# Performance work log

Hardware: AMD Instinct MI355X
Metric: run time of the kernel (lower is better)

## Reference

```python
import jax, jax.numpy as jnp
import numpy as np

B, T, F = 2048, 60, 89
H = 1024
OUT = 30  # output_predicted_chords


def setup_inputs() -> dict:
    key = jax.random.key(0)
    k1, k2, k3, k4 = jax.random.split(key, 4)
    # small init scale keeps the relu-activated recurrence numerically stable
    s = 0.02
    return {
        "x": jax.random.normal(k1, (B, T, F), dtype=jnp.float32),
        "W": jax.random.normal(k2, (F, 4 * H), dtype=jnp.float32) * s,
        "U": jax.random.normal(k3, (H, 4 * H), dtype=jnp.float32) * s,
        "b": jnp.zeros((4 * H,), dtype=jnp.float32),
        "Wd": jax.random.normal(k4, (H, OUT), dtype=jnp.float32) * s,
        "bd": jnp.zeros((OUT,), dtype=jnp.float32),
    }


def _lstm_last_h(x, W, U, b):
    """Keras LSTM(activation='relu', recurrent_activation='sigmoid').
    Gate order in Keras kernels: i, f, c (candidate), o.
    Returns last hidden state h_T of shape [B, H]."""
    Bsz = x.shape[0]
    Hdim = U.shape[0]
    # precompute input projections for all timesteps: [T, B, 4H]
    xz = jnp.einsum('btf,fg->tbg', x, W) + b

    def step(carry, xz_t):
        h, c = carry
        z = xz_t + h @ U                      # [B, 4H]
        i, f, g, o = jnp.split(z, 4, axis=-1)
        i = jax.nn.sigmoid(i)
        f = jax.nn.sigmoid(f)
        g = jax.nn.relu(g)                    # activation='relu' on candidate
        o = jax.nn.sigmoid(o)
        c = f * c + i * g
        h = o * jax.nn.relu(c)                # activation='relu' on cell output
        return (h, c), None

    h0 = jnp.zeros((Bsz, Hdim), dtype=x.dtype)
    c0 = jnp.zeros((Bsz, Hdim), dtype=x.dtype)
    (hT, _), _ = jax.lax.scan(step, (h0, c0), xz)
    return hT


def reference(x, W, U, b, Wd, bd):
    # LSTM(return_sequences=True) then take x[:, -1, :] == last hidden state
    hT = _lstm_last_h(x, W, U, b)             # [B, H]
    y = hT @ Wd + bd                           # [B, OUT]
    return y.reshape(-1, OUT, 1)               # [B, 30, 1]
```

## Files before the change

### kernel.cpp

```cpp
#include <hip/hip_runtime.h>
#include <cstdint>
#include <cstddef>

#define Bsz 2048
#define Tseq 60
#define Fin 89
#define Hd 1024
#define G4 4096
#define KXP 128
#define NOUT 30

typedef _Float16 half8 __attribute__((ext_vector_type(8)));
typedef float f32x4 __attribute__((ext_vector_type(4)));

__device__ __forceinline__ void gload_lds16(const void* g, void* l) {
  __builtin_amdgcn_global_load_lds((const __attribute__((address_space(1))) void*)g,
                                   (__attribute__((address_space(3))) void*)l,
                                   16, 0, 0);
}

__device__ __forceinline__ float sigmoidf_fast(float x) {
  return 1.0f / (1.0f + __expf(-x));
}


__global__ __launch_bounds__(256) void convert_x(const float* __restrict__ x,
                                                 _Float16* __restrict__ xp) {
  int idx = blockIdx.x * 256 + threadIdx.x;
  int k = idx % KXP;
  int b = (idx / KXP) % Bsz;
  int t = idx / (KXP * Bsz);
  float v = (k < Fin) ? x[((size_t)b * Tseq + t) * Fin + k] : 0.0f;
  xp[idx] = (_Float16)v;
}

__global__ __launch_bounds__(256) void transpose_W(const float* __restrict__ W,
                                                   _Float16* __restrict__ Wpt) {
  __shared__ float tile[32][33];
  int n0 = blockIdx.x * 32;
  int k0 = blockIdx.y * 32;
  int tx = threadIdx.x, ty = threadIdx.y;
  for (int i = ty; i < 32; i += 8) {
    int k = k0 + i;
    tile[i][tx] = (k < Fin) ? W[(size_t)k * G4 + n0 + tx] : 0.0f;
  }
  __syncthreads();
  for (int i = ty; i < 32; i += 8)
    Wpt[(size_t)(n0 + i) * KXP + k0 + tx] = (_Float16)tile[tx][i];
}

__global__ __launch_bounds__(256) void transpose_U(const float* __restrict__ U,
                                                   _Float16* __restrict__ Upt) {
  __shared__ float tile[32][33];
  int n0 = blockIdx.x * 32;
  int k0 = blockIdx.y * 32;
  int tx = threadIdx.x, ty = threadIdx.y;
  for (int i = ty; i < 32; i += 8)
    tile[i][tx] = U[(size_t)(k0 + i) * G4 + n0 + tx];
  __syncthreads();
  for (int i = ty; i < 32; i += 8)
    Upt[(size_t)(n0 + i) * Hd + k0 + tx] = (_Float16)tile[tx][i];
}

__global__ __launch_bounds__(256, 2) void lstm_step(
    const _Float16* __restrict__ xp_t,
    const _Float16* __restrict__ Wpt,
    const _Float16* __restrict__ Upt,
    const float*    __restrict__ bias,
    const _Float16* __restrict__ h_in,
    _Float16*       __restrict__ h_out,
    float*          __restrict__ cst,
    int skip_h)
{
  __shared__ __align__(16) _Float16 As[2 * 8192];
  __shared__ __align__(16) _Float16 Bs[2 * 8192];

  const int tid  = threadIdx.x;
  const int wave = tid >> 6;
  const int lane = tid & 63;
  const int quad = lane >> 4;
  const int l16  = lane & 15;

  const int id  = blockIdx.x;
  const int xcd = id & 7, loc = id >> 3;
  const int m0 = (((xcd & 1) << 3) + (loc & 7)) * 128;
  const int j0 = (((xcd >> 1) << 3) + (loc >> 3)) * 32;

  const int srow = lane >> 2;
  const int qg   = (lane & 3) ^ ((lane >> 3) & 3);
  const int sA   = quad ^ ((l16 >> 1) & 3);

  const int hb    = 16 * (wave & 1);
  const int mwave = 64 * (wave >> 1);
  const int j  = j0 + hb + l16;
  const int uA = 4 * (wave >> 1);
  const int uB = wave & 1;
  const int aoff = l16 * 32 + sA * 8;

  float bv[4];
  for (int p = 0; p < 4; ++p) bv[p] = bias[p * Hd + j];

  f32x4 acc[4][4];
  for (int mi = 0; mi < 4; ++mi)
    for (int p = 0; p < 4; ++p)
      acc[mi][p] = f32x4{bv[p], bv[p], bv[p], bv[p]};

  auto stage = [&](int buf, int r) {
    const _Float16* Ab; const _Float16* Bb; int strA, strB, k0;
    if (r < 2) { Ab = xp_t; strA = KXP; Bb = Wpt; strB = KXP; k0 = r * 64; }
    else       { Ab = h_in; strA = Hd;  Bb = Upt; strB = Hd;  k0 = (r - 2) * 64; }
    _Float16* Ad = &As[buf * 8192];
    _Float16* Bd = &Bs[buf * 8192];
#pragma unroll
    for (int ii = 0; ii < 4; ++ii) {
      int i = ii * 4 + wave;
      int st = i >> 3, ci = i & 7;
      gload_lds16(Ab + (size_t)(m0 + ci * 16 + srow) * strA + k0 + st * 32 + qg * 8,
                  Ad + st * 4096 + ci * 512);
    }
#pragma unroll
    for (int ii = 0; ii < 4; ++ii) {
      int i = ii * 4 + wave;
      int st = i >> 3, ci = i & 7;
      int ln = ci * 16 + srow;
      int gn = (ln >> 5) * Hd + j0 + (ln & 31);
      gload_lds16(Bb + (size_t)gn * strB + k0 + st * 32 + qg * 8,
                  Bd + st * 4096 + ci * 512);
    }
  };

  auto compute = [&](int buf) {
    const __attribute__((address_space(3))) _Float16* As3 =
        (const __attribute__((address_space(3))) _Float16*)&As[buf * 8192];
    const __attribute__((address_space(3))) _Float16* Bs3 =
        (const __attribute__((address_space(3))) _Float16*)&Bs[buf * 8192];
    half8 a0[4], b0[4], a1[4], b1[4];
#pragma unroll
    for (int mi = 0; mi < 4; ++mi)
      asm volatile("ds_read_b128 %0, %1" : "=v"(a0[mi])
                   : "v"(As3 + (uA + mi) * 512 + aoff) : "memory");
#pragma unroll
    for (int p = 0; p < 4; ++p)
      asm volatile("ds_read_b128 %0, %1" : "=v"(b0[p])
                   : "v"(Bs3 + (2 * p + uB) * 512 + aoff) : "memory");
#pragma unroll
    for (int mi = 0; mi < 4; ++mi)
      asm volatile("ds_read_b128 %0, %1" : "=v"(a1[mi])
                   : "v"(As3 + 4096 + (uA + mi) * 512 + aoff) : "memory");
#pragma unroll
    for (int p = 0; p < 4; ++p)
      asm volatile("ds_read_b128 %0, %1" : "=v"(b1[p])
                   : "v"(Bs3 + 4096 + (2 * p + uB) * 512 + aoff) : "memory");
    asm volatile("s_waitcnt lgkmcnt(8)" ::: "memory");
    __builtin_amdgcn_sched_barrier(0);
#pragma unroll
    for (int mi = 0; mi < 4; ++mi)
#pragma unroll
      for (int p = 0; p < 4; ++p)
        acc[mi][p] = __builtin_amdgcn_mfma_f32_16x16x32_f16(a0[mi], b0[p],
                                                            acc[mi][p], 0, 0, 0);
    asm volatile("s_waitcnt lgkmcnt(0)" ::: "memory");
    __builtin_amdgcn_sched_barrier(0);
#pragma unroll
    for (int mi = 0; mi < 4; ++mi)
#pragma unroll
      for (int p = 0; p < 4; ++p)
        acc[mi][p] = __builtin_amdgcn_mfma_f32_16x16x32_f16(a1[mi], b1[p],
                                                            acc[mi][p], 0, 0, 0);
  };

  const int NR = skip_h ? 2 : 18;

  stage(0, 0);
  stage(1, 1);
  for (int r = 0; r < NR; ++r) {
    const int cur = r & 1;
    if (r < NR - 1) {
      asm volatile("s_waitcnt vmcnt(8)" ::: "memory");
    } else {
      asm volatile("s_waitcnt vmcnt(0)" ::: "memory");
    }
    __builtin_amdgcn_sched_barrier(0);
    __builtin_amdgcn_s_barrier();
    __builtin_amdgcn_s_setprio(1);
    compute(cur);
    __builtin_amdgcn_s_setprio(0);
    __builtin_amdgcn_s_barrier();
    if (r + 2 < NR) stage(cur, r + 2);
  }

  for (int mi = 0; mi < 4; ++mi) {
    for (int r = 0; r < 4; ++r) {
      int row = m0 + mwave + mi * 16 + quad * 4 + r;
      size_t idx = (size_t)row * Hd + j;
      float iv = sigmoidf_fast(acc[mi][0][r]);
      float fv = sigmoidf_fast(acc[mi][1][r]);
      float gv = fmaxf(acc[mi][2][r], 0.0f);
      float ov = sigmoidf_fast(acc[mi][3][r]);
      float cprev = skip_h ? 0.0f : cst[idx];
      float cv = fv * cprev + iv * gv;
      cst[idx] = cv;
      float hv = ov * fmaxf(cv, 0.0f);
      h_out[idx] = (_Float16)hv;
    }
  }
}

__global__ __launch_bounds__(256) void final_dense(const _Float16* __restrict__ h,
                                                   const float* __restrict__ Wd,
                                                   const float* __restrict__ bd,
                                                   float* __restrict__ y) {
  __shared__ float hs[Hd];
  __shared__ float red[8][32];
  int bi = blockIdx.x;
  for (int k = threadIdx.x; k < Hd; k += 256)
    hs[k] = (float)h[(size_t)bi * Hd + k];
  __syncthreads();
  int o  = threadIdx.x & 31;
  int ch = threadIdx.x >> 5;
  float p = 0.0f;
  if (o < NOUT) {
    int k0 = ch * (Hd / 8);
    for (int k = k0; k < k0 + (Hd / 8); ++k)
      p += hs[k] * Wd[(size_t)k * NOUT + o];
  }
  red[ch][o] = p;
  __syncthreads();
  if (threadIdx.x < NOUT) {
    float s = bd[threadIdx.x];
    for (int c2 = 0; c2 < 8; ++c2) s += red[c2][threadIdx.x];
    y[(size_t)bi * NOUT + threadIdx.x] = s;
  }
}


extern "C" void kernel_launch(void* const* d_in, const int* in_sizes, int n_in,
                              void* d_out, int out_size, void* d_ws, size_t ws_size,
                              hipStream_t stream) {
  const float* x  = (const float*)d_in[0];
  const float* W  = (const float*)d_in[1];
  const float* U  = (const float*)d_in[2];
  const float* b  = (const float*)d_in[3];
  const float* Wd = (const float*)d_in[4];
  const float* bd = (const float*)d_in[5];
  float* y = (float*)d_out;

  char* ws = (char*)d_ws;
  _Float16* xp  = (_Float16*)ws; ws += (size_t)Tseq * Bsz * KXP * 2;
  _Float16* Wpt = (_Float16*)ws; ws += (size_t)G4 * KXP * 2;
  _Float16* Upt = (_Float16*)ws; ws += (size_t)G4 * Hd * 2;
  _Float16* hb0 = (_Float16*)ws; ws += (size_t)Bsz * Hd * 2;
  _Float16* hb1 = (_Float16*)ws; ws += (size_t)Bsz * Hd * 2;
  float*    cst = (float*)ws;    ws += (size_t)Bsz * Hd * 4;

  convert_x<<<(Tseq * Bsz * KXP) / 256, 256, 0, stream>>>(x, xp);
  transpose_W<<<dim3(G4 / 32, KXP / 32), dim3(32, 8), 0, stream>>>(W, Wpt);
  transpose_U<<<dim3(G4 / 32, Hd / 32), dim3(32, 8), 0, stream>>>(U, Upt);

  for (int t = 0; t < Tseq; ++t) {
    const _Float16* hin  = ((t - 1) & 1) ? hb1 : hb0;
    _Float16*       hout = (t & 1) ? hb1 : hb0;
    lstm_step<<<dim3((Bsz / 128) * (G4 / 128)), 256, 0, stream>>>(
        xp + (size_t)t * (Bsz * KXP), Wpt, Upt, b,
        (t == 0) ? hb0 : hin, hout, cst, (t == 0) ? 1 : 0);
  }

  final_dense<<<Bsz, 256, 0, stream>>>(hb1, Wd, bd, y);
}
```

Before: 1.723 ms.

## Enlarge LSTM step tile to 128x256 with 8 waves and triple-buffered LDS

Each block now computes a 128-row by 256-gate-column tile (64 hidden units times 4 gates) with 512 threads, halving the grid to 256 blocks. The B operand tile doubles, so each A tile loaded into LDS is reused across twice as many columns. The LDS pipeline moves from double to triple buffering, with vmcnt waits adjusted to the new in-flight load counts. This cuts redundant global reads of h and x per step and gives the loads more latency hiding. In exchange it needs more LDS per block (144 KB), allows only one block per CU, and leaves 256 blocks for the machine's CUs, so wave-level parallelism is lower.

```diff
diff --git a/kernel.cpp b/kernel.cpp
--- a/kernel.cpp
+++ b/kernel.cpp
@@ -62,7 +62,7 @@
     Upt[(size_t)(n0 + i) * Hd + k0 + tx] = (_Float16)tile[tx][i];
 }
 
-__global__ __launch_bounds__(256, 2) void lstm_step(
+__global__ __launch_bounds__(512, 1) void lstm_step(
     const _Float16* __restrict__ xp_t,
     const _Float16* __restrict__ Wpt,
     const _Float16* __restrict__ Upt,
@@ -72,8 +72,8 @@
     float*          __restrict__ cst,
     int skip_h)
 {
-  __shared__ __align__(16) _Float16 As[2 * 8192];
-  __shared__ __align__(16) _Float16 Bs[2 * 8192];
+  __shared__ __align__(16) _Float16 As[3 * 8192];
+  __shared__ __align__(16) _Float16 Bs[3 * 16384];
 
   const int tid  = threadIdx.x;
   const int wave = tid >> 6;
@@ -83,25 +83,28 @@
 
   const int id  = blockIdx.x;
   const int xcd = id & 7, loc = id >> 3;
-  const int m0 = (((xcd & 1) << 3) + (loc & 7)) * 128;
-  const int j0 = (((xcd >> 1) << 3) + (loc >> 3)) * 32;
+  const int jpanel = 4 * (xcd & 3) + (loc & 3);
+  const int mpanel = 8 * (xcd >> 2) + (loc >> 2);
+  const int m0 = mpanel * 128;
+  const int j0 = jpanel * 64;
 
   const int srow = lane >> 2;
   const int qg   = (lane & 3) ^ ((lane >> 3) & 3);
   const int sA   = quad ^ ((l16 >> 1) & 3);
 
-  const int hb    = 16 * (wave & 1);
-  const int mwave = 64 * (wave >> 1);
-  const int j  = j0 + hb + l16;
-  const int uA = 4 * (wave >> 1);
-  const int uB = wave & 1;
+  const int mhalf = wave >> 2;
+  const int nq    = wave & 3;
+  const int j  = j0 + 16 * nq + l16;
   const int aoff = l16 * 32 + sA * 8;
 
   float bv[4];
+#pragma unroll
   for (int p = 0; p < 4; ++p) bv[p] = bias[p * Hd + j];
 
   f32x4 acc[4][4];
+#pragma unroll
   for (int mi = 0; mi < 4; ++mi)
+#pragma unroll
     for (int p = 0; p < 4; ++p)
       acc[mi][p] = f32x4{bv[p], bv[p], bv[p], bv[p]};
 
@@ -110,22 +113,21 @@
     if (r < 2) { Ab = xp_t; strA = KXP; Bb = Wpt; strB = KXP; k0 = r * 64; }
     else       { Ab = h_in; strA = Hd;  Bb = Upt; strB = Hd;  k0 = (r - 2) * 64; }
     _Float16* Ad = &As[buf * 8192];
-    _Float16* Bd = &Bs[buf * 8192];
-#pragma unroll
-    for (int ii = 0; ii < 4; ++ii) {
-      int i = ii * 4 + wave;
+    _Float16* Bd = &Bs[buf * 16384];
+#pragma unroll
+    for (int ii = 0; ii < 2; ++ii) {
+      int i = ii * 8 + wave;
       int st = i >> 3, ci = i & 7;
       gload_lds16(Ab + (size_t)(m0 + ci * 16 + srow) * strA + k0 + st * 32 + qg * 8,
                   Ad + st * 4096 + ci * 512);
     }
 #pragma unroll
     for (int ii = 0; ii < 4; ++ii) {
-      int i = ii * 4 + wave;
-      int st = i >> 3, ci = i & 7;
-      int ln = ci * 16 + srow;
-      int gn = (ln >> 5) * Hd + j0 + (ln & 31);
+      int i = ii * 8 + wave;
+      int st = i >> 4, ci = i & 15;
+      int gn = (ci >> 2) * Hd + j0 + 16 * (ci & 3) + srow;
       gload_lds16(Bb + (size_t)gn * strB + k0 + st * 32 + qg * 8,
-                  Bd + st * 4096 + ci * 512);
+                  Bd + st * 8192 + ci * 512);
     }
   };
 
@@ -133,24 +135,24 @@
     const __attribute__((address_space(3))) _Float16* As3 =
         (const __attribute__((address_space(3))) _Float16*)&As[buf * 8192];
     const __attribute__((address_space(3))) _Float16* Bs3 =
-        (const __attribute__((address_space(3))) _Float16*)&Bs[buf * 8192];
+        (const __attribute__((address_space(3))) _Float16*)&Bs[buf * 16384];
     half8 a0[4], b0[4], a1[4], b1[4];
 #pragma unroll
     for (int mi = 0; mi < 4; ++mi)
       asm volatile("ds_read_b128 %0, %1" : "=v"(a0[mi])
-                   : "v"(As3 + (uA + mi) * 512 + aoff) : "memory");
+                   : "v"(As3 + (4 * mhalf + mi) * 512 + aoff) : "memory");
 #pragma unroll
     for (int p = 0; p < 4; ++p)
       asm volatile("ds_read_b128 %0, %1" : "=v"(b0[p])
-                   : "v"(Bs3 + (2 * p + uB) * 512 + aoff) : "memory");
+                   : "v"(Bs3 + (4 * p + nq) * 512 + aoff) : "memory");
 #pragma unroll
     for (int mi = 0; mi < 4; ++mi)
       asm volatile("ds_read_b128 %0, %1" : "=v"(a1[mi])
-                   : "v"(As3 + 4096 + (uA + mi) * 512 + aoff) : "memory");
+                   : "v"(As3 + 4096 + (4 * mhalf + mi) * 512 + aoff) : "memory");
 #pragma unroll
     for (int p = 0; p < 4; ++p)
       asm volatile("ds_read_b128 %0, %1" : "=v"(b1[p])
-                   : "v"(Bs3 + 4096 + (2 * p + uB) * 512 + aoff) : "memory");
+                   : "v"(Bs3 + 8192 + (4 * p + nq) * 512 + aoff) : "memory");
     asm volatile("s_waitcnt lgkmcnt(8)" ::: "memory");
     __builtin_amdgcn_sched_barrier(0);
 #pragma unroll
@@ -173,30 +175,32 @@
 
   stage(0, 0);
   stage(1, 1);
+  if (NR > 2) stage(2, 2);
+
   for (int r = 0; r < NR; ++r) {
-    const int cur = r & 1;
-    if (r < NR - 1) {
-      asm volatile("s_waitcnt vmcnt(8)" ::: "memory");
-    } else {
-      asm volatile("s_waitcnt vmcnt(0)" ::: "memory");
-    }
+    const int cur = r % 3;
+    if (NR - r >= 3)      asm volatile("s_waitcnt vmcnt(12)" ::: "memory");
+    else if (NR - r == 2) asm volatile("s_waitcnt vmcnt(6)"  ::: "memory");
+    else                  asm volatile("s_waitcnt vmcnt(0)"  ::: "memory");
     __builtin_amdgcn_sched_barrier(0);
     __builtin_amdgcn_s_barrier();
     __builtin_amdgcn_s_setprio(1);
     compute(cur);
     __builtin_amdgcn_s_setprio(0);
     __builtin_amdgcn_s_barrier();
-    if (r + 2 < NR) stage(cur, r + 2);
-  }
-
+    if (r + 3 < NR) stage(cur, r + 3);
+  }
+
+#pragma unroll
   for (int mi = 0; mi < 4; ++mi) {
-    for (int r = 0; r < 4; ++r) {
-      int row = m0 + mwave + mi * 16 + quad * 4 + r;
+#pragma unroll
+    for (int rr = 0; rr < 4; ++rr) {
+      int row = m0 + 64 * mhalf + mi * 16 + quad * 4 + rr;
       size_t idx = (size_t)row * Hd + j;
-      float iv = sigmoidf_fast(acc[mi][0][r]);
-      float fv = sigmoidf_fast(acc[mi][1][r]);
-      float gv = fmaxf(acc[mi][2][r], 0.0f);
-      float ov = sigmoidf_fast(acc[mi][3][r]);
+      float iv = sigmoidf_fast(acc[mi][0][rr]);
+      float fv = sigmoidf_fast(acc[mi][1][rr]);
+      float gv = fmaxf(acc[mi][2][rr], 0.0f);
+      float ov = sigmoidf_fast(acc[mi][3][rr]);
       float cprev = skip_h ? 0.0f : cst[idx];
       float cv = fv * cprev + iv * gv;
       cst[idx] = cv;
@@ -260,7 +264,7 @@
   for (int t = 0; t < Tseq; ++t) {
     const _Float16* hin  = ((t - 1) & 1) ? hb1 : hb0;
     _Float16*       hout = (t & 1) ? hb1 : hb0;
-    lstm_step<<<dim3((Bsz / 128) * (G4 / 128)), 256, 0, stream>>>(
+    lstm_step<<<dim3((Bsz / 128) * (G4 / 256)), 512, 0, stream>>>(
         xp + (size_t)t * (Bsz * KXP), Wpt, Upt, b,
         (t == 0) ? hb0 : hin, hout, cst, (t == 0) ? 1 : 0);
   }
```

Measured after the change: 1.865 ms. +8.3%, slower.
